# Performance work log

Measured on AMD Instinct MI355X. Metric: run time of the kernel, lower is better.

Reference implementation:

```python
import jax, jax.numpy as jnp
import numpy as np

B, S, E, H = 2, 2048, 1024, 16
HD = E // H  # head_dim = 64


def setup_inputs() -> dict:
    key = jax.random.key(0)
    k_x, k_wqkv, k_bqkv, k_wo, k_bo = jax.random.split(key, 5)
    # nn.Linear-style init scale ~ 1/sqrt(fan_in)
    s = 1.0 / np.sqrt(E)
    return {
        "x": jax.random.normal(k_x, (B, S, E), dtype=jnp.float32),
        "W_qkv": jax.random.uniform(k_wqkv, (3 * E, E), jnp.float32, -s, s),
        "b_qkv": jax.random.uniform(k_bqkv, (3 * E,), jnp.float32, -s, s),
        "W_out": jax.random.uniform(k_wo, (E, E), jnp.float32, -s, s),
        "b_out": jax.random.uniform(k_bo, (E,), jnp.float32, -s, s),
    }


def reference(x, W_qkv, b_qkv, W_out, b_out):
    # Fused QKV projection: (B,S,E) -> (B,S,3E)
    qkv = jnp.einsum("bse,fe->bsf", x, W_qkv) + b_qkv
    # Faithful to the torch code: reshape to (B,S,H,3*HD), then chunk last dim.
    qkv = qkv.reshape(B, S, H, 3 * HD)
    q, k, v = jnp.split(qkv, 3, axis=-1)  # each (B,S,H,HD)
    scale = 1.0 / jnp.sqrt(jnp.asarray(HD, dtype=x.dtype))
    # scores: (B,H,S,S)
    scores = jnp.einsum("bshd,bthd->bhst", q, k) * scale
    weights = jax.nn.softmax(scores, axis=-1)
    # context: (B,S,H,HD) -> (B,S,E)
    ctx = jnp.einsum("bhst,bthd->bshd", weights, v).reshape(B, S, E)
    return jnp.einsum("bse,fe->bsf", ctx, W_out) + b_out
```

## Files before the change

### kernel.cpp

```cpp
#include <hip/hip_runtime.h>
#include <hip/hip_bf16.h>

#define B_  2
#define S_  2048
#define E_  1024
#define H_  16
#define HD_ 64
#define T_  (B_*S_)
#define F_  (3*E_)

#define SW(r) ((((r) & 7) << 4) ^ (((r) & 8) << 2))

using bf16 = __hip_bfloat16;
typedef __attribute__((ext_vector_type(8))) short bf16x8;
typedef __attribute__((ext_vector_type(4))) float f32x4;
typedef __attribute__((ext_vector_type(16))) float f32x16;
typedef __attribute__((ext_vector_type(4))) int i32x4;
typedef __attribute__((ext_vector_type(2))) unsigned int u32x2;

__device__ inline short f2bf(float x) {
  __hip_bfloat16 h = __float2bfloat16(x);
  return __builtin_bit_cast(short, h);
}
__device__ inline float bf2f(short x) {
  return __bfloat162float(__builtin_bit_cast(__hip_bfloat16, x));
}
__device__ inline int pk2(float lo, float hig) {
  return (int)((unsigned short)f2bf(lo) |
               ((unsigned int)(unsigned short)f2bf(hig) << 16));
}

__device__ inline void gload_lds16(const void* g, void* l) {
  __builtin_amdgcn_global_load_lds(
      (const __attribute__((address_space(1))) void*)g,
      (__attribute__((address_space(3))) void*)l, 16, 0, 0);
}

__global__ __launch_bounds__(256) void cvt_f32_bf16(
    const float* __restrict__ in, short* __restrict__ out, int n8) {
  int i = blockIdx.x * 256 + threadIdx.x;
  if (i >= n8) return;
  const float4* p = (const float4*)in + (size_t)i * 2;
  float4 a = p[0], b = p[1];
  bf16x8 r;
  r[0] = f2bf(a.x); r[1] = f2bf(a.y); r[2] = f2bf(a.z); r[3] = f2bf(a.w);
  r[4] = f2bf(b.x); r[5] = f2bf(b.y); r[6] = f2bf(b.z); r[7] = f2bf(b.w);
  *(bf16x8*)(out + (size_t)i * 8) = r;
}

__device__ inline void store_out(short* p, float v) { *p = f2bf(v); }
__device__ inline void store_out(float* p, float v) { *p = v; }

template<typename OutT>
__global__ __launch_bounds__(256) void gemm_nt(
    const short* __restrict__ A,
    const short* __restrict__ Bm,
    const float* __restrict__ bias,
    OutT* __restrict__ C,
    int M, int N, int K) {
  __shared__ __align__(16) char sAB[32768];
  char* sA = sAB;
  char* sB = sAB + 16384;
  const int tid  = threadIdx.x;
  const int w    = tid >> 6, lane = tid & 63;
  const int lr   = lane & 15, g = lane >> 4;
  const int brow = blockIdx.y * 128, bcol = blockIdx.x * 128;
  const int wr   = (w >> 1) * 64,  wc   = (w & 1) * 64;

  f32x4 acc[4][4];
  #pragma unroll
  for (int i = 0; i < 4; ++i)
    #pragma unroll
    for (int j = 0; j < 4; ++j) acc[i][j] = (f32x4)0.0f;

  const size_t Kb = (size_t)K * 2;
  const char* Ag = (const char*)A + (size_t)brow * Kb;
  const char* Bg = (const char*)Bm + (size_t)bcol * Kb;

  for (int k0 = 0; k0 < K; k0 += 64) {
    #pragma unroll
    for (int i = 0; i < 4; ++i) {
      int base = i * 4096 + w * 1024;
      int lb   = base + lane * 16;
      int r    = lb >> 7;
      int cb   = (lb & 127) ^ ((r & 7) << 4);
      gload_lds16(Ag + (size_t)r * Kb + (size_t)k0 * 2 + cb, sA + base);
      gload_lds16(Bg + (size_t)r * Kb + (size_t)k0 * 2 + cb, sB + base);
    }
    __syncthreads();
    #pragma unroll
    for (int ks = 0; ks < 2; ++ks) {
      bf16x8 af[4], bfr[4];
      #pragma unroll
      for (int m = 0; m < 4; ++m) {
        int row = wr + m * 16 + lr;
        int cb  = (ks * 64 + g * 16) ^ ((row & 7) << 4);
        af[m] = *(const bf16x8*)(sA + row * 128 + cb);
      }
      #pragma unroll
      for (int n = 0; n < 4; ++n) {
        int row = wc + n * 16 + lr;
        int cb  = (ks * 64 + g * 16) ^ ((row & 7) << 4);
        bfr[n] = *(const bf16x8*)(sB + row * 128 + cb);
      }
      #pragma unroll
      for (int m = 0; m < 4; ++m)
        #pragma unroll
        for (int n = 0; n < 4; ++n)
          acc[m][n] = __builtin_amdgcn_mfma_f32_16x16x32_bf16(
              af[m], bfr[n], acc[m][n], 0, 0, 0);
    }
    __syncthreads();
  }
  #pragma unroll
  for (int n = 0; n < 4; ++n) {
    int f = bcol + wc + n * 16 + lr;
    float bv = bias[f];
    #pragma unroll
    for (int m = 0; m < 4; ++m) {
      int t0 = brow + wr + m * 16 + g * 4;
      #pragma unroll
      for (int j = 0; j < 4; ++j) {
        store_out(&C[(size_t)(t0 + j) * N + f], acc[m][n][j] + bv);
      }
    }
  }
}

__global__ __launch_bounds__(128) void attn_kernel(
    const short* __restrict__ qkv, short* __restrict__ ctx) {
  __shared__ __align__(16) char smem[32768];
  const int tid = threadIdx.x;
  const int w = tid >> 6, lane = tid & 63;
  const int ql = lane & 31, hi = lane >> 5;
  const int qblk = blockIdx.x, h = blockIdx.y, b = blockIdx.z;

  const size_t rowB = (size_t)F_ * 2;
  const char* base = (const char*)qkv + (size_t)b * S_ * rowB + (size_t)h * 384;

  const int qrow = qblk * 64 + w * 32 + ql;
  const char* qp = base + (size_t)qrow * rowB;
  bf16x8 qf[4];
  #pragma unroll
  for (int ks = 0; ks < 4; ++ks) {
    bf16x8 t = *(const bf16x8*)(qp + ks * 32 + hi * 16);
    #pragma unroll
    for (int j = 0; j < 8; ++j) t[j] = f2bf(bf2f(t[j]) * 0.180336880f);
    qf[ks] = t;
  }

  const int vkg = tid & 15;
  const int vfg = (tid >> 4) & 7;

  float m_run = -3.0e38f, l_run = 0.0f;
  f32x16 ot0 = (f32x16)0.0f, ot1 = (f32x16)0.0f;

#define STAGE_K(dstoff, srcb)                                           \
  do {                                                                  \
    _Pragma("unroll")                                                   \
    for (int i = 0; i < 4; ++i) {                                       \
      int ubase = i * 2048 + w * 1024;                                  \
      int lb = ubase + lane * 16;                                       \
      int r  = lb >> 7;                                                 \
      int cb = (lb & 127) ^ SW(r);                                      \
      gload_lds16((srcb) + (size_t)r * rowB + 128 + cb,                 \
                  smem + (dstoff) + ubase);                             \
    }                                                                   \
  } while (0)

#define LOAD_V(srcb)                                                    \
  do {                                                                  \
    const char* vp_ = (srcb) + 256 + vfg * 16;                          \
    nv0 = *(const bf16x8*)(vp_ + (size_t)(vkg * 4 + 0) * rowB);         \
    nv1 = *(const bf16x8*)(vp_ + (size_t)(vkg * 4 + 1) * rowB);         \
    nv2 = *(const bf16x8*)(vp_ + (size_t)(vkg * 4 + 2) * rowB);         \
    nv3 = *(const bf16x8*)(vp_ + (size_t)(vkg * 4 + 3) * rowB);         \
  } while (0)

#define WRITE_VT(dstoff)                                                \
  do {                                                                  \
    char* dvt_ = smem + (dstoff) + 8192;                                \
    _Pragma("unroll")                                                   \
    for (int f = 0; f < 8; ++f) {                                       \
      int fr = vfg * 8 + f;                                             \
      u32x2 dw;                                                         \
      dw[0] = (unsigned short)nv0[f] |                                  \
              ((unsigned int)(unsigned short)nv1[f] << 16);             \
      dw[1] = (unsigned short)nv2[f] |                                  \
              ((unsigned int)(unsigned short)nv3[f] << 16);             \
      *(u32x2*)(dvt_ + fr * 128 + ((vkg * 8) ^ SW(fr))) = dw;           \
    }                                                                   \
  } while (0)

  {
    bf16x8 nv0, nv1, nv2, nv3;
    STAGE_K(0, base);
    LOAD_V(base);
    WRITE_VT(0);
  }
  __syncthreads();

  int cur = 0;
  for (int kt = 0; kt < 32; ++kt) {
    const int nxt = cur ^ 1;
    const char* sK  = smem + cur * 16384;
    const char* sVt = sK + 8192;

    bf16x8 nv0, nv1, nv2, nv3;
    const char* nkvb = base + (size_t)((kt + 1) * 64) * rowB;
    if (kt < 31) {
      STAGE_K(nxt * 16384, nkvb);
      LOAD_V(nkvb);
    }

    f32x16 st0 = (f32x16)0.0f, st1 = (f32x16)0.0f;
    __builtin_amdgcn_s_setprio(1);
    #pragma unroll
    for (int ks = 0; ks < 4; ++ks) {
      int cb = (ks * 32 + hi * 16) ^ SW(ql);
      bf16x8 k0 = *(const bf16x8*)(sK + ql * 128 + cb);
      bf16x8 k1 = *(const bf16x8*)(sK + (ql + 32) * 128 + cb);
      st0 = __builtin_amdgcn_mfma_f32_32x32x16_bf16(k0, qf[ks], st0, 0, 0, 0);
      st1 = __builtin_amdgcn_mfma_f32_32x32x16_bf16(k1, qf[ks], st1, 0, 0, 0);
    }
    __builtin_amdgcn_s_setprio(0);

    float mx = fmaxf(st0[0], st1[0]);
    #pragma unroll
    for (int r = 1; r < 16; ++r) mx = fmaxf(mx, fmaxf(st0[r], st1[r]));
    mx = fmaxf(mx, __shfl_xor(mx, 32));
    if (!__all(mx <= m_run + 8.0f)) {
      float mn = fmaxf(m_run, mx);
      float al = exp2f(m_run - mn);
      m_run = mn;
      l_run *= al;
      #pragma unroll
      for (int r = 0; r < 16; ++r) { ot0[r] *= al; ot1[r] *= al; }
    }
    float p0[16], p1[16];
    float rs = 0.0f;
    #pragma unroll
    for (int r = 0; r < 16; ++r) {
      p0[r] = exp2f(st0[r] - m_run);
      p1[r] = exp2f(st1[r] - m_run);
      rs += p0[r] + p1[r];
    }
    rs += __shfl_xor(rs, 32);
    l_run += rs;

    int pa[8], pb[8], pc[8], pd[8];
    #pragma unroll
    for (int r = 0; r < 8; ++r) pa[r] = pk2(p0[2 * r], p0[2 * r + 1]);
    #pragma unroll
    for (int r = 0; r < 8; ++r) pb[r] = __shfl_xor(pa[r], 32);
    #pragma unroll
    for (int r = 0; r < 8; ++r) pc[r] = pk2(p1[2 * r], p1[2 * r + 1]);
    #pragma unroll
    for (int r = 0; r < 8; ++r) pd[r] = __shfl_xor(pc[r], 32);
    i32x4 paw[4];
    paw[0][0] = hi ? pb[2] : pa[0];  paw[0][1] = hi ? pb[3] : pa[1];
    paw[0][2] = hi ? pa[2] : pb[0];  paw[0][3] = hi ? pa[3] : pb[1];
    paw[1][0] = hi ? pb[6] : pa[4];  paw[1][1] = hi ? pb[7] : pa[5];
    paw[1][2] = hi ? pa[6] : pb[4];  paw[1][3] = hi ? pa[7] : pb[5];
    paw[2][0] = hi ? pd[2] : pc[0];  paw[2][1] = hi ? pd[3] : pc[1];
    paw[2][2] = hi ? pc[2] : pd[0];  paw[2][3] = hi ? pc[3] : pd[1];
    paw[3][0] = hi ? pd[6] : pc[4];  paw[3][1] = hi ? pd[7] : pc[5];
    paw[3][2] = hi ? pc[6] : pd[4];  paw[3][3] = hi ? pc[7] : pd[5];

    __builtin_amdgcn_s_setprio(1);
    #pragma unroll
    for (int ks = 0; ks < 4; ++ks) {
      int cb = (ks * 32 + hi * 16) ^ SW(ql);
      bf16x8 pf = __builtin_bit_cast(bf16x8, paw[ks]);
      bf16x8 v0 = *(const bf16x8*)(sVt + ql * 128 + cb);
      bf16x8 v1 = *(const bf16x8*)(sVt + (ql + 32) * 128 + cb);
      ot0 = __builtin_amdgcn_mfma_f32_32x32x16_bf16(v0, pf, ot0, 0, 0, 0);
      ot1 = __builtin_amdgcn_mfma_f32_32x32x16_bf16(v1, pf, ot1, 0, 0, 0);
    }
    __builtin_amdgcn_s_setprio(0);

    if (kt < 31) {
      WRITE_VT(nxt * 16384);
    }
    __syncthreads();
    cur = nxt;
  }

  float inv = 1.0f / l_run;
  short* crow = ctx + ((size_t)b * S_ + qrow) * E_ + h * 64;
  #pragma unroll
  for (int i = 0; i < 8; ++i) {
    int f0 = ((2 * i) & 3) + 8 * (i >> 1) + 4 * hi;
    int w0 = pk2(ot0[2 * i] * inv, ot0[2 * i + 1] * inv);
    int w1 = pk2(ot1[2 * i] * inv, ot1[2 * i + 1] * inv);
    *(int*)(crow + f0)      = w0;
    *(int*)(crow + f0 + 32) = w1;
  }
#undef STAGE_K
#undef LOAD_V
#undef WRITE_VT
}

extern "C" void kernel_launch(void* const* d_in, const int* in_sizes, int n_in,
                              void* d_out, int out_size, void* d_ws, size_t ws_size,
                              hipStream_t stream) {
  const float* x    = (const float*)d_in[0];
  const float* Wqkv = (const float*)d_in[1];
  const float* bqkv = (const float*)d_in[2];
  const float* Wout = (const float*)d_in[3];
  const float* bout = (const float*)d_in[4];

  char* ws = (char*)d_ws;
  short* xb    = (short*)(ws);
  short* wqkvb = (short*)(ws + 8388608);
  short* woutb = (short*)(ws + 8388608 + 6291456);
  short* qkvb  = (short*)(ws + 16777216);
  short* ctx   = (short*)(ws + 16777216 + 25165824);

  cvt_f32_bf16<<<2048, 256, 0, stream>>>(x, xb, (T_ * E_) / 8);
  cvt_f32_bf16<<<1536, 256, 0, stream>>>(Wqkv, wqkvb, (F_ * E_) / 8);
  cvt_f32_bf16<<<512, 256, 0, stream>>>(Wout, woutb, (E_ * E_) / 8);

  gemm_nt<short><<<dim3(F_ / 128, T_ / 128), 256, 0, stream>>>(
      xb, wqkvb, bqkv, qkvb, T_, F_, E_);

  attn_kernel<<<dim3(S_ / 64, H_, B_), 128, 0, stream>>>(qkvb, ctx);

  gemm_nt<float><<<dim3(E_ / 128, T_ / 128), 256, 0, stream>>>(
      ctx, woutb, bout, (float*)d_out, T_, E_, E_);
}
```

Before: 237.9 us.

## Split attention KV range across two wave groups and swizzle GEMM block order

The attention kernel now uses 512-thread blocks covering 128 query rows, with two groups of four waves each handling half of the key/value sequence. The two partial softmax states are merged through shared memory at the end. The intent is to share the K/V tile staging among more query rows and give more waves per block to hide latency, at the cost of 64KB of LDS per block, an extra merge step and fewer blocks in the grid. The GEMM also remaps block IDs in groups of 8, which appears aimed at XCD-aware scheduling for better L2 locality.

```diff
diff --git a/kernel.cpp b/kernel.cpp
--- a/kernel.cpp
+++ b/kernel.cpp
@@ -13,6 +13,7 @@
 
 using bf16 = __hip_bfloat16;
 typedef __attribute__((ext_vector_type(8))) short bf16x8;
+typedef __attribute__((ext_vector_type(4))) short short4v;
 typedef __attribute__((ext_vector_type(4))) float f32x4;
 typedef __attribute__((ext_vector_type(16))) float f32x16;
 typedef __attribute__((ext_vector_type(4))) int i32x4;
@@ -64,7 +65,12 @@
   const int tid  = threadIdx.x;
   const int w    = tid >> 6, lane = tid & 63;
   const int lr   = lane & 15, g = lane >> 4;
-  const int brow = blockIdx.y * 128, bcol = blockIdx.x * 128;
+  const int nwg  = gridDim.x * gridDim.y;
+  const int bid  = blockIdx.y * gridDim.x + blockIdx.x;
+  const int cpx  = nwg >> 3;
+  const int swz  = (bid & 7) * cpx + (bid >> 3);
+  const int bxs  = swz % gridDim.x, bys = swz / gridDim.x;
+  const int brow = bys * 128, bcol = bxs * 128;
   const int wr   = (w >> 1) * 64,  wc   = (w & 1) * 64;
 
   f32x4 acc[4][4];
@@ -127,18 +133,19 @@
   }
 }
 
-__global__ __launch_bounds__(128) void attn_kernel(
+__global__ __launch_bounds__(512) void attn_kernel(
     const short* __restrict__ qkv, short* __restrict__ ctx) {
-  __shared__ __align__(16) char smem[32768];
+  __shared__ __align__(16) char smem[65536];
   const int tid = threadIdx.x;
   const int w = tid >> 6, lane = tid & 63;
+  const int wq = w & 3, ws = w >> 2;
   const int ql = lane & 31, hi = lane >> 5;
   const int qblk = blockIdx.x, h = blockIdx.y, b = blockIdx.z;
 
   const size_t rowB = (size_t)F_ * 2;
   const char* base = (const char*)qkv + (size_t)b * S_ * rowB + (size_t)h * 384;
 
-  const int qrow = qblk * 64 + w * 32 + ql;
+  const int qrow = qblk * 128 + wq * 32 + ql;
   const char* qp = base + (size_t)qrow * rowB;
   bf16x8 qf[4];
   #pragma unroll
@@ -149,8 +156,10 @@
     qf[ks] = t;
   }
 
-  const int vkg = tid & 15;
-  const int vfg = (tid >> 4) & 7;
+  const int ht  = tid & 255;
+  const int vkg = ht & 15;
+  const int vfg = ht >> 4;
+  const int soff = ws * 32768;
 
   float m_run = -3.0e38f, l_run = 0.0f;
   f32x16 ot0 = (f32x16)0.0f, ot1 = (f32x16)0.0f;
@@ -158,8 +167,8 @@
 #define STAGE_K(dstoff, srcb)                                           \
   do {                                                                  \
     _Pragma("unroll")                                                   \
-    for (int i = 0; i < 4; ++i) {                                       \
-      int ubase = i * 2048 + w * 1024;                                  \
+    for (int i = 0; i < 2; ++i) {                                       \
+      int ubase = i * 4096 + wq * 1024;                                 \
       int lb = ubase + lane * 16;                                       \
       int r  = lb >> 7;                                                 \
       int cb = (lb & 127) ^ SW(r);                                      \
@@ -170,19 +179,19 @@
 
 #define LOAD_V(srcb)                                                    \
   do {                                                                  \
-    const char* vp_ = (srcb) + 256 + vfg * 16;                          \
-    nv0 = *(const bf16x8*)(vp_ + (size_t)(vkg * 4 + 0) * rowB);         \
-    nv1 = *(const bf16x8*)(vp_ + (size_t)(vkg * 4 + 1) * rowB);         \
-    nv2 = *(const bf16x8*)(vp_ + (size_t)(vkg * 4 + 2) * rowB);         \
-    nv3 = *(const bf16x8*)(vp_ + (size_t)(vkg * 4 + 3) * rowB);         \
+    const char* vp_ = (srcb) + 256 + vfg * 8;                           \
+    nv0 = *(const short4v*)(vp_ + (size_t)(vkg * 4 + 0) * rowB);        \
+    nv1 = *(const short4v*)(vp_ + (size_t)(vkg * 4 + 1) * rowB);        \
+    nv2 = *(const short4v*)(vp_ + (size_t)(vkg * 4 + 2) * rowB);        \
+    nv3 = *(const short4v*)(vp_ + (size_t)(vkg * 4 + 3) * rowB);        \
   } while (0)
 
 #define WRITE_VT(dstoff)                                                \
   do {                                                                  \
     char* dvt_ = smem + (dstoff) + 8192;                                \
     _Pragma("unroll")                                                   \
-    for (int f = 0; f < 8; ++f) {                                       \
-      int fr = vfg * 8 + f;                                             \
+    for (int f = 0; f < 4; ++f) {                                       \
+      int fr = vfg * 4 + f;                                             \
       u32x2 dw;                                                         \
       dw[0] = (unsigned short)nv0[f] |                                  \
               ((unsigned int)(unsigned short)nv1[f] << 16);             \
@@ -193,23 +202,24 @@
   } while (0)
 
   {
-    bf16x8 nv0, nv1, nv2, nv3;
-    STAGE_K(0, base);
-    LOAD_V(base);
-    WRITE_VT(0);
+    short4v nv0, nv1, nv2, nv3;
+    const char* kvb0 = base + (size_t)(ws * 1024) * rowB;
+    STAGE_K(soff, kvb0);
+    LOAD_V(kvb0);
+    WRITE_VT(soff);
   }
   __syncthreads();
 
   int cur = 0;
-  for (int kt = 0; kt < 32; ++kt) {
+  for (int kt = 0; kt < 16; ++kt) {
     const int nxt = cur ^ 1;
-    const char* sK  = smem + cur * 16384;
+    const char* sK  = smem + soff + cur * 16384;
     const char* sVt = sK + 8192;
 
-    bf16x8 nv0, nv1, nv2, nv3;
-    const char* nkvb = base + (size_t)((kt + 1) * 64) * rowB;
-    if (kt < 31) {
-      STAGE_K(nxt * 16384, nkvb);
+    short4v nv0, nv1, nv2, nv3;
+    const char* nkvb = base + (size_t)(ws * 1024 + (kt + 1) * 64) * rowB;
+    if (kt < 15) {
+      STAGE_K(soff + nxt * 16384, nkvb);
       LOAD_V(nkvb);
     }
 
@@ -279,22 +289,50 @@
     }
     __builtin_amdgcn_s_setprio(0);
 
-    if (kt < 31) {
-      WRITE_VT(nxt * 16384);
+    if (kt < 15) {
+      WRITE_VT(soff + nxt * 16384);
     }
     __syncthreads();
     cur = nxt;
   }
 
-  float inv = 1.0f / l_run;
-  short* crow = ctx + ((size_t)b * S_ + qrow) * E_ + h * 64;
-  #pragma unroll
-  for (int i = 0; i < 8; ++i) {
-    int f0 = ((2 * i) & 3) + 8 * (i >> 1) + 4 * hi;
-    int w0 = pk2(ot0[2 * i] * inv, ot0[2 * i + 1] * inv);
-    int w1 = pk2(ot1[2 * i] * inv, ot1[2 * i + 1] * inv);
-    *(int*)(crow + f0)      = w0;
-    *(int*)(crow + f0 + 32) = w1;
+  float* sc = (float*)smem + (size_t)(wq * 64 + lane) * 36;
+  if (ws == 1) {
+    #pragma unroll
+    for (int i = 0; i < 4; ++i) {
+      f32x4 t0 = {ot0[4 * i], ot0[4 * i + 1], ot0[4 * i + 2], ot0[4 * i + 3]};
+      f32x4 t1 = {ot1[4 * i], ot1[4 * i + 1], ot1[4 * i + 2], ot1[4 * i + 3]};
+      *(f32x4*)(sc + 4 * i)      = t0;
+      *(f32x4*)(sc + 16 + 4 * i) = t1;
+    }
+    sc[32] = m_run;
+    sc[33] = l_run;
+  }
+  __syncthreads();
+  if (ws == 0) {
+    float mb = sc[32], lb = sc[33];
+    float mn = fmaxf(m_run, mb);
+    float aa = exp2f(m_run - mn), ab = exp2f(mb - mn);
+    float linv = 1.0f / (l_run * aa + lb * ab);
+    float ob0[16], ob1[16];
+    #pragma unroll
+    for (int i = 0; i < 4; ++i) {
+      f32x4 t0 = *(const f32x4*)(sc + 4 * i);
+      f32x4 t1 = *(const f32x4*)(sc + 16 + 4 * i);
+      #pragma unroll
+      for (int j = 0; j < 4; ++j) { ob0[4 * i + j] = t0[j]; ob1[4 * i + j] = t1[j]; }
+    }
+    short* crow = ctx + ((size_t)b * S_ + qrow) * E_ + h * 64;
+    #pragma unroll
+    for (int i = 0; i < 8; ++i) {
+      int f0 = ((2 * i) & 3) + 8 * (i >> 1) + 4 * hi;
+      float a0 = (ot0[2 * i]     * aa + ob0[2 * i]     * ab) * linv;
+      float a1 = (ot0[2 * i + 1] * aa + ob0[2 * i + 1] * ab) * linv;
+      float b0 = (ot1[2 * i]     * aa + ob1[2 * i]     * ab) * linv;
+      float b1 = (ot1[2 * i + 1] * aa + ob1[2 * i + 1] * ab) * linv;
+      *(int*)(crow + f0)      = pk2(a0, a1);
+      *(int*)(crow + f0 + 32) = pk2(b0, b1);
+    }
   }
 #undef STAGE_K
 #undef LOAD_V
@@ -324,7 +362,7 @@
   gemm_nt<short><<<dim3(F_ / 128, T_ / 128), 256, 0, stream>>>(
       xb, wqkvb, bqkv, qkvb, T_, F_, E_);
 
-  attn_kernel<<<dim3(S_ / 64, H_, B_), 128, 0, stream>>>(qkvb, ctx);
+  attn_kernel<<<dim3(S_ / 128, H_, B_), 512, 0, stream>>>(qkvb, ctx);
 
   gemm_nt<float><<<dim3(E_ / 128, T_ / 128), 256, 0, stream>>>(
       ctx, woutb, bout, (float*)d_out, T_, E_, E_);
```

Measured after the change: 242.5 us. Within noise of the previous version (+1.9%).

## Widen attention blocks to 128 queries and add 128x64 tile output GEMM

Applied to the files above, without the earlier changes.

The attention kernel now runs four waves per block, each covering 32 query rows, so each staged K/V tile is shared by 128 queries instead of 64. The K staging and V transpose work is split across twice as many threads, with narrower per-thread V loads. A new output-projection GEMM uses 128x64 tiles, which doubles the block count for the E×E projection to improve occupancy and load balance. Trade-offs are fewer attention blocks (512), more registers and contention per block, and lower reuse per block in the new GEMM.

```diff
diff --git a/kernel.cpp b/kernel.cpp
--- a/kernel.cpp
+++ b/kernel.cpp
@@ -13,6 +13,7 @@
 
 using bf16 = __hip_bfloat16;
 typedef __attribute__((ext_vector_type(8))) short bf16x8;
+typedef __attribute__((ext_vector_type(4))) short short4v;
 typedef __attribute__((ext_vector_type(4))) float f32x4;
 typedef __attribute__((ext_vector_type(16))) float f32x16;
 typedef __attribute__((ext_vector_type(4))) int i32x4;
@@ -127,7 +128,88 @@
   }
 }
 
-__global__ __launch_bounds__(128) void attn_kernel(
+__global__ __launch_bounds__(256) void gemm_nt_n64(
+    const short* __restrict__ A,
+    const short* __restrict__ Bm,
+    const float* __restrict__ bias,
+    float* __restrict__ C,
+    int M, int N, int K) {
+  __shared__ __align__(16) char sAB[24576];
+  char* sA = sAB;
+  char* sB = sAB + 16384;
+  const int tid  = threadIdx.x;
+  const int w    = tid >> 6, lane = tid & 63;
+  const int lr   = lane & 15, g = lane >> 4;
+  const int brow = blockIdx.y * 128, bcol = blockIdx.x * 64;
+
+  f32x4 acc[2][4];
+  #pragma unroll
+  for (int i = 0; i < 2; ++i)
+    #pragma unroll
+    for (int j = 0; j < 4; ++j) acc[i][j] = (f32x4)0.0f;
+
+  const size_t Kb = (size_t)K * 2;
+  const char* Ag = (const char*)A + (size_t)brow * Kb;
+  const char* Bg = (const char*)Bm + (size_t)bcol * Kb;
+
+  for (int k0 = 0; k0 < K; k0 += 64) {
+    #pragma unroll
+    for (int i = 0; i < 4; ++i) {
+      int base = i * 4096 + w * 1024;
+      int lb   = base + lane * 16;
+      int r    = lb >> 7;
+      int cb   = (lb & 127) ^ ((r & 7) << 4);
+      gload_lds16(Ag + (size_t)r * Kb + (size_t)k0 * 2 + cb, sA + base);
+    }
+    #pragma unroll
+    for (int i = 0; i < 2; ++i) {
+      int base = i * 4096 + w * 1024;
+      int lb   = base + lane * 16;
+      int r    = lb >> 7;
+      int cb   = (lb & 127) ^ ((r & 7) << 4);
+      gload_lds16(Bg + (size_t)r * Kb + (size_t)k0 * 2 + cb, sB + base);
+    }
+    __syncthreads();
+    #pragma unroll
+    for (int ks = 0; ks < 2; ++ks) {
+      bf16x8 af[2], bfr[4];
+      #pragma unroll
+      for (int m = 0; m < 2; ++m) {
+        int row = w * 32 + m * 16 + lr;
+        int cb  = (ks * 64 + g * 16) ^ ((row & 7) << 4);
+        af[m] = *(const bf16x8*)(sA + row * 128 + cb);
+      }
+      #pragma unroll
+      for (int n = 0; n < 4; ++n) {
+        int row = n * 16 + lr;
+        int cb  = (ks * 64 + g * 16) ^ ((row & 7) << 4);
+        bfr[n] = *(const bf16x8*)(sB + row * 128 + cb);
+      }
+      #pragma unroll
+      for (int m = 0; m < 2; ++m)
+        #pragma unroll
+        for (int n = 0; n < 4; ++n)
+          acc[m][n] = __builtin_amdgcn_mfma_f32_16x16x32_bf16(
+              af[m], bfr[n], acc[m][n], 0, 0, 0);
+    }
+    __syncthreads();
+  }
+  #pragma unroll
+  for (int n = 0; n < 4; ++n) {
+    int f = bcol + n * 16 + lr;
+    float bv = bias[f];
+    #pragma unroll
+    for (int m = 0; m < 2; ++m) {
+      int t0 = brow + w * 32 + m * 16 + g * 4;
+      #pragma unroll
+      for (int j = 0; j < 4; ++j) {
+        C[(size_t)(t0 + j) * N + f] = acc[m][n][j] + bv;
+      }
+    }
+  }
+}
+
+__global__ __launch_bounds__(256) void attn_kernel(
     const short* __restrict__ qkv, short* __restrict__ ctx) {
   __shared__ __align__(16) char smem[32768];
   const int tid = threadIdx.x;
@@ -138,7 +220,7 @@
   const size_t rowB = (size_t)F_ * 2;
   const char* base = (const char*)qkv + (size_t)b * S_ * rowB + (size_t)h * 384;
 
-  const int qrow = qblk * 64 + w * 32 + ql;
+  const int qrow = qblk * 128 + w * 32 + ql;
   const char* qp = base + (size_t)qrow * rowB;
   bf16x8 qf[4];
   #pragma unroll
@@ -150,7 +232,7 @@
   }
 
   const int vkg = tid & 15;
-  const int vfg = (tid >> 4) & 7;
+  const int vfg = tid >> 4;
 
   float m_run = -3.0e38f, l_run = 0.0f;
   f32x16 ot0 = (f32x16)0.0f, ot1 = (f32x16)0.0f;
@@ -158,31 +240,31 @@
 #define STAGE_K(dstoff, srcb)                                           \
   do {                                                                  \
     _Pragma("unroll")                                                   \
-    for (int i = 0; i < 4; ++i) {                                       \
-      int ubase = i * 2048 + w * 1024;                                  \
-      int lb = ubase + lane * 16;                                       \
+    for (int i = 0; i < 2; ++i) {                                       \
+      int lbase = i * 4096 + w * 1024;                                  \
+      int lb = lbase + lane * 16;                                       \
       int r  = lb >> 7;                                                 \
       int cb = (lb & 127) ^ SW(r);                                      \
       gload_lds16((srcb) + (size_t)r * rowB + 128 + cb,                 \
-                  smem + (dstoff) + ubase);                             \
+                  smem + (dstoff) + lbase);                             \
     }                                                                   \
   } while (0)
 
 #define LOAD_V(srcb)                                                    \
   do {                                                                  \
-    const char* vp_ = (srcb) + 256 + vfg * 16;                          \
-    nv0 = *(const bf16x8*)(vp_ + (size_t)(vkg * 4 + 0) * rowB);         \
-    nv1 = *(const bf16x8*)(vp_ + (size_t)(vkg * 4 + 1) * rowB);         \
-    nv2 = *(const bf16x8*)(vp_ + (size_t)(vkg * 4 + 2) * rowB);         \
-    nv3 = *(const bf16x8*)(vp_ + (size_t)(vkg * 4 + 3) * rowB);         \
+    const char* vp_ = (srcb) + 256 + vfg * 8;                           \
+    nv0 = *(const short4v*)(vp_ + (size_t)(vkg * 4 + 0) * rowB);        \
+    nv1 = *(const short4v*)(vp_ + (size_t)(vkg * 4 + 1) * rowB);        \
+    nv2 = *(const short4v*)(vp_ + (size_t)(vkg * 4 + 2) * rowB);        \
+    nv3 = *(const short4v*)(vp_ + (size_t)(vkg * 4 + 3) * rowB);        \
   } while (0)
 
 #define WRITE_VT(dstoff)                                                \
   do {                                                                  \
     char* dvt_ = smem + (dstoff) + 8192;                                \
     _Pragma("unroll")                                                   \
-    for (int f = 0; f < 8; ++f) {                                       \
-      int fr = vfg * 8 + f;                                             \
+    for (int f = 0; f < 4; ++f) {                                       \
+      int fr = vfg * 4 + f;                                             \
       u32x2 dw;                                                         \
       dw[0] = (unsigned short)nv0[f] |                                  \
               ((unsigned int)(unsigned short)nv1[f] << 16);             \
@@ -193,7 +275,7 @@
   } while (0)
 
   {
-    bf16x8 nv0, nv1, nv2, nv3;
+    short4v nv0, nv1, nv2, nv3;
     STAGE_K(0, base);
     LOAD_V(base);
     WRITE_VT(0);
@@ -206,7 +288,7 @@
     const char* sK  = smem + cur * 16384;
     const char* sVt = sK + 8192;
 
-    bf16x8 nv0, nv1, nv2, nv3;
+    short4v nv0, nv1, nv2, nv3;
     const char* nkvb = base + (size_t)((kt + 1) * 64) * rowB;
     if (kt < 31) {
       STAGE_K(nxt * 16384, nkvb);
@@ -324,8 +406,8 @@
   gemm_nt<short><<<dim3(F_ / 128, T_ / 128), 256, 0, stream>>>(
       xb, wqkvb, bqkv, qkvb, T_, F_, E_);
 
-  attn_kernel<<<dim3(S_ / 64, H_, B_), 128, 0, stream>>>(qkvb, ctx);
-
-  gemm_nt<float><<<dim3(E_ / 128, T_ / 128), 256, 0, stream>>>(
+  attn_kernel<<<dim3(S_ / 128, H_, B_), 256, 0, stream>>>(qkvb, ctx);
+
+  gemm_nt_n64<<<dim3(E_ / 64, T_ / 128), 256, 0, stream>>>(
       ctx, woutb, bout, (float*)d_out, T_, E_, E_);
 }
```

New measurement: 228.5 us. -4.0%, faster.
